# Kernel optimization log

Hardware: AMD Instinct MI355X
Metric: run time of the kernel (lower is better)

The kernel has to match this reference:

```python
import jax, jax.numpy as jnp
import numpy as np

N_E = 1024
E_DIM = 256
BETA = 0.25
DECAY = 0.99
EPS = 1e-5


def setup_inputs() -> dict:
    key = jax.random.key(0)
    k1, k2 = jax.random.split(key)
    z = jax.random.normal(k1, (16, E_DIM, 64, 64), dtype=jnp.float32)
    # embedding.weight.data.uniform_(-1/n_e, 1/n_e)
    weight = jax.random.uniform(k2, (N_E, E_DIM), dtype=jnp.float32,
                                minval=-1.0 / N_E, maxval=1.0 / N_E)
    cluster_size = jnp.zeros((N_E,), dtype=jnp.float32)
    embedding_avg = weight  # clone of initial weight
    return {"z": z, "weight": weight, "cluster_size": cluster_size,
            "embedding_avg": embedding_avg}


def reference(z, weight, cluster_size, embedding_avg):
    B, C, H, W = z.shape  # C == e_dim
    zp = jnp.transpose(z, (0, 2, 3, 1))          # [B,H,W,C]
    zf = zp.reshape(-1, C)                       # [N, C], N = B*H*W

    # ||z||^2 + ||e||^2 - 2 z e^T  -> [N, n_e]
    d = (jnp.sum(zf * zf, axis=1, keepdims=True)
         + jnp.sum(weight * weight, axis=1)
         - 2.0 * jnp.matmul(zf, weight.T))
    idx = jnp.argmin(d, axis=1)                  # [N] int

    z_q = weight[idx].reshape(zp.shape)          # [B,H,W,C]

    # EMA codebook update (training branch), computed with scatter-sums
    n_e = weight.shape[0]
    counts = jax.ops.segment_sum(jnp.ones(zf.shape[0], dtype=zf.dtype),
                                 idx, num_segments=n_e)        # encodings.sum(0)
    new_cluster_size = cluster_size * DECAY + (1.0 - DECAY) * counts
    n = jnp.sum(new_cluster_size)
    cs_smoothed = (new_cluster_size + EPS) / (n + n_e * EPS) * n
    dw = jax.ops.segment_sum(zf, idx, num_segments=n_e)        # encodings.T @ zf
    new_embedding_avg = embedding_avg * DECAY + (1.0 - DECAY) * dw
    new_weight = new_embedding_avg / cs_smoothed[:, None]

    loss = BETA * jnp.mean((jax.lax.stop_gradient(z_q) - zp) ** 2)
    z_q_st = zp + jax.lax.stop_gradient(z_q - zp)   # straight-through
    out = jnp.transpose(z_q_st, (0, 3, 1, 2))        # back to NCHW
    return out, loss, idx, new_cluster_size, new_embedding_avg, new_weight
```

## Files before the change

### kernel.cpp

```cpp
#include <hip/hip_runtime.h>
#include <hip/hip_bf16.h>

typedef unsigned short ushort_t;
typedef __attribute__((ext_vector_type(8))) _Float16 half8;
typedef __attribute__((ext_vector_type(4))) _Float16 half4;
typedef __attribute__((ext_vector_type(4))) float f32x4;

#define NB    16
#define NC    256
#define NHW   4096
#define NPIX  65536
#define NE    1024
#define BETA  0.25f
#define DECAY 0.99f
#define EPS_  1e-5f
#define GAP_FLAG 1.25e-4f

#define OFF_LOSS 16777216
#define OFF_IDXF 16777217
#define OFF_NCS  16842753
#define OFF_NEA  16843777
#define OFF_NW   17105921

#define WS_WSUM  0
#define WS_CSSM  1024
#define WS_LPART 2048
#define WS_CNT   4096
#define WS_FLAGS 4128
#define WS_LIST  6176
#define WS_WF16  40960
#define WS_ZF16  (WS_WF16 + 131072)
#define WS_IDXI  (WS_ZF16 + 8388608)
#define WS_CCNT  (WS_IDXI + 65536)
#define WS_OFFS  (WS_CCNT + 1024)
#define WS_CUR   (WS_OFFS + 1024)
#define WS_SORT  (WS_CUR + 1024)
#define WS_END   (WS_SORT + 65536)

__device__ __forceinline__ float sq_nofma(float x) {
    float s = x * x;
    asm volatile("" : "+v"(s));
    return s;
}

__device__ __forceinline__ float np_pair128_sq(const float* __restrict__ a) {
    float r[8];
    #pragma unroll
    for (int m = 0; m < 8; ++m) r[m] = sq_nofma(a[m]);
    for (int i = 8; i < 128; i += 8) {
        #pragma unroll
        for (int m = 0; m < 8; ++m) r[m] += sq_nofma(a[i + m]);
    }
    return ((r[0] + r[1]) + (r[2] + r[3])) + ((r[4] + r[5]) + (r[6] + r[7]));
}

__device__ __forceinline__ void gload16(const void* g, void* ldsp) {
    __builtin_amdgcn_global_load_lds((const __attribute__((address_space(1))) unsigned int*)g,
                                     (__attribute__((address_space(3))) unsigned int*)ldsp,
                                     16, 0, 0);
}

__global__ __launch_bounds__(64) void wsum_kernel(const float* __restrict__ w,
                                                  float* __restrict__ wsum,
                                                  float* __restrict__ ncs,
                                                  int* __restrict__ cnt,
                                                  int* __restrict__ ccount,
                                                  float* __restrict__ lpart) {
    int j = blockIdx.x * 64 + threadIdx.x;
    const float* wr = w + (size_t)j * NC;
    wsum[j] = np_pair128_sq(wr) + np_pair128_sq(wr + 128);
    ncs[j] = 0.0f;
    ccount[j] = 0;
    lpart[j] = 0.0f;
    lpart[j + 1024] = 0.0f;
    if (j == 0) cnt[0] = 0;
}

__global__ __launch_bounds__(256) void wpack_kernel(const float* __restrict__ w,
                                                    _Float16* __restrict__ wf) {
    int i = blockIdx.x * 256 + threadIdx.x;
    wf[i] = (_Float16)(w[i] * 1024.0f);
}

__global__ __launch_bounds__(256) void zpack_kernel(const float* __restrict__ z,
                                                    _Float16* __restrict__ zf) {
    __shared__ float zs[64 * 65];
    const int t = threadIdx.x;
    const int P0 = blockIdx.x * 64;
    const int b = P0 >> 12, hw0 = P0 & (NHW - 1);
    const int K0 = blockIdx.y * 64;
    const int hw = t & 63, cq = t >> 6;
    const float* zb = z + (size_t)b * (NC * NHW) + hw0 + hw;
    #pragma unroll
    for (int i = 0; i < 16; ++i) {
        int kl = cq * 16 + i;
        zs[hw * 65 + kl] = zb[(size_t)(K0 + kl) * NHW];
    }
    __syncthreads();
    const int p = t >> 2, kq = t & 3;
    size_t obase = (size_t)(P0 + p) * NC + K0 + kq * 16;
    #pragma unroll
    for (int h2 = 0; h2 < 2; ++h2) {
        half8 v;
        #pragma unroll
        for (int j2 = 0; j2 < 8; ++j2)
            v[j2] = (_Float16)zs[p * 65 + kq * 16 + h2 * 8 + j2];
        *(half8*)&zf[obase + h2 * 8] = v;
    }
}

__global__ __launch_bounds__(256) void gemm2_kernel(const _Float16* __restrict__ wf,
                                                    const _Float16* __restrict__ zf,
                                                    const float* __restrict__ wsum,
                                                    float* __restrict__ idxf,
                                                    int* __restrict__ idxi,
                                                    ushort_t* __restrict__ list,
                                                    int* __restrict__ cnt,
                                                    float* __restrict__ ncs,
                                                    int* __restrict__ ccount) {
    __shared__ __align__(16) char smem[81920];
    _Float16* zt = (_Float16*)smem;
    _Float16* wt = (_Float16*)(smem + 65536);
    float* bvx = (float*)(smem + 65536);
    float* svx = bvx + 256;
    int*   bix = (int*)(svx + 256);
    int*   h   = (int*)smem;

    const int t = threadIdx.x;
    const int l = t & 63;
    const int w = t >> 6;
    const int P0 = blockIdx.x * 128;
    const int wc = w >> 1, wp = w & 1;

    auto stage_w = [&](int ct, int ks, int buf) {
        #pragma unroll
        for (int i = 0; i < 2; ++i) {
            int row = w * 32 + i * 16 + (l >> 2);
            int gc = (l & 3) ^ ((l >> 3) & 3);
            gload16(wf + (size_t)(ct * 128 + row) * NC + ks * 32 + gc * 8,
                    &wt[buf * 4096 + w * 1024 + i * 512 + l * 8]);
        }
    };

    #pragma unroll
    for (int i = 0; i < 16; ++i) {
        int row = w * 32 + i * 2 + (l >> 5);
        int gc = (l & 31) ^ (row & 7);
        gload16(zf + (size_t)(P0 + row) * NC + gc * 8,
                &zt[w * 8192 + i * 512 + l * 8]);
    }
    stage_w(0, 0, 0);

    float rbv2[4], rsv2[4];
    int   rbi2[4];
    #pragma unroll
    for (int n = 0; n < 4; ++n) { rbv2[n] = 3.4e38f; rsv2[n] = 3.4e38f; rbi2[n] = 0; }

    __syncthreads();

    int buf = 0;
    for (int ct = 0; ct < 8; ++ct) {
        f32x4 acc[4][4];
        #pragma unroll
        for (int m = 0; m < 4; ++m)
            #pragma unroll
            for (int n = 0; n < 4; ++n)
                #pragma unroll
                for (int e = 0; e < 4; ++e) acc[m][n][e] = 0.0f;

        for (int ks = 0; ks < 8; ++ks) {
            int step = ct * 8 + ks;
            if (step < 63) {
                int ns = step + 1;
                stage_w(ns >> 3, ns & 7, buf ^ 1);
            }
            half8 a[4], b[4];
            #pragma unroll
            for (int m = 0; m < 4; ++m) {
                int row = wc * 64 + m * 16 + (l & 15);
                int g = (l >> 4) ^ ((row >> 1) & 3);
                a[m] = *(const half8*)&wt[buf * 4096 + row * 32 + g * 8];
            }
            #pragma unroll
            for (int n = 0; n < 4; ++n) {
                int row = wp * 64 + n * 16 + (l & 15);
                int chunk = (ks * 4 + (l >> 4)) ^ (row & 7);
                b[n] = *(const half8*)&zt[row * 256 + chunk * 8];
            }
            #pragma unroll
            for (int m = 0; m < 4; ++m)
                #pragma unroll
                for (int n = 0; n < 4; ++n)
                    acc[m][n] = __builtin_amdgcn_mfma_f32_16x16x32_f16(a[m], b[n], acc[m][n], 0, 0, 0);
            __syncthreads();
            buf ^= 1;
        }

        #pragma unroll
        for (int m = 0; m < 4; ++m) {
            float4 env = *(const float4*)&wsum[ct * 128 + wc * 64 + m * 16 + (l >> 4) * 4];
            const float* en = &env.x;
            #pragma unroll
            for (int n = 0; n < 4; ++n)
                #pragma unroll
                for (int r = 0; r < 4; ++r) {
                    float s = en[r] - acc[m][n][r] * 0.001953125f;
                    int code = ct * 128 + wc * 64 + m * 16 + (l >> 4) * 4 + r;
                    if (s < rbv2[n]) { rsv2[n] = rbv2[n]; rbv2[n] = s; rbi2[n] = code; }
                    else if (s < rsv2[n]) rsv2[n] = s;
                }
        }
    }

    #pragma unroll
    for (int n = 0; n < 4; ++n) {
        float bv = rbv2[n], sv = rsv2[n];
        int bi = rbi2[n];
        #pragma unroll
        for (int x = 16; x <= 32; x <<= 1) {
            float v2 = __shfl_xor(bv, x);
            float s2 = __shfl_xor(sv, x);
            int   i2 = __shfl_xor(bi, x);
            if (v2 < bv || (v2 == bv && i2 < bi)) { sv = fminf(bv, s2); bv = v2; bi = i2; }
            else sv = fminf(sv, v2);
        }
        if ((l >> 4) == 0) {
            int lp = wp * 64 + n * 16 + l;
            bvx[wc * 128 + lp] = bv;
            svx[wc * 128 + lp] = sv;
            bix[wc * 128 + lp] = bi;
        }
    }
    #pragma unroll
    for (int e = 0; e < 4; ++e) h[t + e * 256] = 0;
    __syncthreads();
    if (t < 128) {
        float bv = bvx[t], sv = svx[t];
        int bi = bix[t];
        float v2 = bvx[128 + t], s2 = svx[128 + t];
        int i2 = bix[128 + t];
        if (v2 < bv || (v2 == bv && i2 < bi)) { sv = fminf(bv, s2); bv = v2; bi = i2; }
        else sv = fminf(sv, v2);
        int pix = P0 + t;
        idxf[pix] = (float)bi;
        idxi[pix] = bi;
        atomicAdd(&h[bi], 1);
        if (sv - bv < GAP_FLAG) {
            int pos = atomicAdd(cnt, 1);
            list[pos] = (ushort_t)pix;
        }
    }
    __syncthreads();
    #pragma unroll
    for (int e = 0; e < 4; ++e) {
        int v = h[t + e * 256];
        if (v) {
            atomicAdd(&ncs[t + e * 256], (float)v);
            atomicAdd(&ccount[t + e * 256], v);
        }
    }
}

__global__ __launch_bounds__(256) void argmin_kernel(const float* __restrict__ z,
                                                     const float* __restrict__ w,
                                                     const float* __restrict__ enorm,
                                                     float* __restrict__ idxf,
                                                     int* __restrict__ idxi,
                                                     unsigned long long* __restrict__ flags) {
    __shared__ __align__(16) float smem[64 * 68 + 128 * 68];
    float* zt = smem;
    float* wt = smem + 64 * 68;
    const int t = threadIdx.x;
    const int pr = t & 7;
    const int cr = t >> 3;
    const int P0 = blockIdx.x * 64;
    const int b = P0 >> 12;
    const int hw0 = P0 & (NHW - 1);
    const float* zb = z + (size_t)b * (NC * NHW) + hw0;
    float bestv[8], secv[8];
    int besti[8];
    #pragma unroll
    for (int i = 0; i < 8; ++i) { bestv[i] = 3.4e38f; secv[i] = 3.4e38f; besti[i] = 0; }
    for (int cc = 0; cc < 8; ++cc) {
        float acc[8][4];
        #pragma unroll
        for (int i = 0; i < 8; ++i)
            #pragma unroll
            for (int j = 0; j < 4; ++j) acc[i][j] = 0.0f;
        for (int kc = 0; kc < 4; ++kc) {
            {
                int p = t & 63;
                int k0 = (t >> 6) * 16;
                int f2 = ((p >> 3) & 3) << 2;
                #pragma unroll
                for (int i = 0; i < 16; ++i) {
                    int k = k0 + i;
                    zt[p * 68 + (k ^ f2)] = zb[(size_t)(kc * 64 + k) * NHW + p];
                }
            }
            {
                #pragma unroll
                for (int i = 0; i < 8; ++i) {
                    int f = t + 256 * i;
                    int jj = f >> 4;
                    int k4 = f & 15;
                    float4 v = *(const float4*)&w[(size_t)(cc * 128 + jj) * NC + kc * 64 + k4 * 4];
                    *(float4*)&wt[jj * 68 + k4 * 4] = v;
                }
            }
            __syncthreads();
            #pragma unroll 2
            for (int k = 0; k < 64; k += 4) {
                float4 za[8], wb[4];
                #pragma unroll
                for (int i = 0; i < 8; ++i)
                    za[i] = *(float4*)&zt[(pr + 8 * i) * 68 + (k ^ ((i & 3) << 2))];
                #pragma unroll
                for (int j = 0; j < 4; ++j)
                    wb[j] = *(float4*)&wt[(cr + 32 * j) * 68 + k];
                #pragma unroll
                for (int i = 0; i < 8; ++i)
                    #pragma unroll
                    for (int j = 0; j < 4; ++j)
                        acc[i][j] += za[i].x * wb[j].x + za[i].y * wb[j].y +
                                     za[i].z * wb[j].z + za[i].w * wb[j].w;
            }
            __syncthreads();
        }
        #pragma unroll
        for (int j = 0; j < 4; ++j) {
            int code = cc * 128 + cr + 32 * j;
            float enj = enorm[code];
            #pragma unroll
            for (int i = 0; i < 8; ++i) {
                float s = enj - 2.0f * acc[i][j];
                if (s < bestv[i]) { secv[i] = bestv[i]; bestv[i] = s; besti[i] = code; }
                else if (s < secv[i]) secv[i] = s;
            }
        }
    }
    float* rv = smem;
    int* ri = (int*)(smem + 2048);
    float* rs = smem + 4096;
    #pragma unroll
    for (int i = 0; i < 8; ++i) {
        int p = pr + 8 * i;
        rv[p * 32 + cr] = bestv[i];
        ri[p * 32 + cr] = besti[i];
        rs[p * 32 + cr] = secv[i];
    }
    __syncthreads();
    if (t < 64) {
        int p = t;
        float bv = rv[p * 32], sv = rs[p * 32];
        int bi = ri[p * 32];
        for (int s2 = 1; s2 < 32; ++s2) {
            float v = rv[p * 32 + s2];
            float v2 = rs[p * 32 + s2];
            int ii = ri[p * 32 + s2];
            if (v < bv) { sv = bv; bv = v; bi = ii; }
            else {
                if (v < sv) sv = v;
                if (v == bv && ii < bi) bi = ii;
            }
            if (v2 < sv) sv = v2;
        }
        idxf[P0 + p] = (float)bi;
        idxi[P0 + p] = bi;
        unsigned long long mask = __ballot((sv - bv) < GAP_FLAG);
        if (t == 0) flags[blockIdx.x] = mask;
    }
}

__global__ __launch_bounds__(256) void gather_kernel(const unsigned long long* __restrict__ flags,
                                                     ushort_t* __restrict__ list,
                                                     int* __restrict__ cnt) {
    int p = blockIdx.x * 256 + threadIdx.x;
    unsigned long long m = flags[p >> 6];
    if ((m >> (p & 63)) & 1ULL) {
        int pos = atomicAdd(cnt, 1);
        list[pos] = (ushort_t)p;
    }
}

__global__ __launch_bounds__(1024) void hist_kernel(const int* __restrict__ idxi,
                                                    float* __restrict__ ncs) {
    __shared__ int h[NE];
    int t = threadIdx.x;
    h[t] = 0;
    __syncthreads();
    int gid = blockIdx.x * 1024 + t;
    #pragma unroll
    for (int i = 0; i < 4; ++i) atomicAdd(&h[idxi[gid + i * 16384]], 1);
    __syncthreads();
    if (h[t]) atomicAdd(&ncs[t], (float)h[t]);
}

__global__ __launch_bounds__(1024, 8) void dwloss_kernel(const float* __restrict__ z,
                                                         const float* __restrict__ w,
                                                         const int* __restrict__ idxi,
                                                         float* __restrict__ dw0,
                                                         float* __restrict__ dw1,
                                                         float* __restrict__ lpart) {
    __shared__ float acc[NE];
    __shared__ float wcol[NE];
    __shared__ float ls[16];
    const int c = blockIdx.x;
    const int part = blockIdx.y;
    const int t = threadIdx.x;
    acc[t] = 0.0f;
    wcol[t] = w[(size_t)t * NC + c];
    __syncthreads();
    const float* zc = z + (size_t)c * NHW;
    float lsum = 0.0f;
    #pragma unroll
    for (int half = 0; half < 2; ++half) {
        float4 zv[4];
        int4   iv[4];
        #pragma unroll
        for (int i = 0; i < 4; ++i) {
            int b = part * 8 + half * 4 + i;
            zv[i] = *(const float4*)&zc[(size_t)b * (NC * NHW) + t * 4];
            iv[i] = *(const int4*)&idxi[b * 4096 + t * 4];
        }
        #pragma unroll
        for (int i = 0; i < 4; ++i) {
            float q0 = wcol[iv[i].x], q1 = wcol[iv[i].y];
            float q2 = wcol[iv[i].z], q3 = wcol[iv[i].w];
            float d0 = q0 - zv[i].x, d1 = q1 - zv[i].y;
            float d2 = q2 - zv[i].z, d3 = q3 - zv[i].w;
            lsum += d0 * d0 + d1 * d1 + d2 * d2 + d3 * d3;
            atomicAdd(&acc[iv[i].x], zv[i].x);
            atomicAdd(&acc[iv[i].y], zv[i].y);
            atomicAdd(&acc[iv[i].z], zv[i].z);
            atomicAdd(&acc[iv[i].w], zv[i].w);
        }
    }
    #pragma unroll
    for (int off = 32; off > 0; off >>= 1) lsum += __shfl_down(lsum, off);
    if ((t & 63) == 0) ls[t >> 6] = lsum;
    __syncthreads();
    if (t == 0) {
        float s = 0.0f;
        #pragma unroll
        for (int q = 0; q < 16; ++q) s += ls[q];
        lpart[c * 2 + part] = s;
    }
    float* dwp = part ? dw1 : dw0;
    dwp[(size_t)t * NC + c] = acc[t];
}

__global__ __launch_bounds__(256) void fixup3_kernel(const float* __restrict__ z,
                                                     const float* __restrict__ w,
                                                     const float* __restrict__ wsum,
                                                     const ushort_t* __restrict__ list,
                                                     const int* __restrict__ cnt,
                                                     float* __restrict__ idxf,
                                                     int* __restrict__ idxi,
                                                     float* __restrict__ ncs,
                                                     int* __restrict__ ccount) {
    const int count = cnt[0];
    if (count == 0) return;
    const int ngroups = (count + 7) >> 3;
    const int t = threadIdx.x;

    __shared__ __align__(16) char smem_raw[16384 + 8192];
    double (*zd)[NC] = (double(*)[NC])smem_raw;
    float  (*zf)[NC] = (float(*)[NC])(smem_raw + 16384);
    float* rbv = (float*)(smem_raw + 16384);
    int*   rbi = (int*)smem_raw;
    __shared__ float zs_sh[8];
    __shared__ int   pix_sh[8];
    __shared__ float r2v[8][32];
    __shared__ int   r2i[8][32];

    for (int g = blockIdx.x; g < ngroups; g += gridDim.x) {
        if (t < 8) {
            int i = g * 8 + t;
            pix_sh[t] = (i < count) ? (int)list[i] : (int)list[0];
        }
        __syncthreads();
        #pragma unroll
        for (int px = 0; px < 8; ++px) {
            int p = pix_sh[px];
            int b = p >> 12, hw = p & (NHW - 1);
            float zv = z[(size_t)b * (NC * NHW) + (size_t)t * NHW + hw];
            zf[px][t] = zv;
            zd[px][t] = (double)zv;
        }
        __syncthreads();
        if (t < 8) zs_sh[t] = np_pair128_sq(zf[t]) + np_pair128_sq(zf[t] + 128);
        __syncthreads();

        float zs_reg[8];
        #pragma unroll
        for (int px = 0; px < 8; ++px) zs_reg[px] = zs_sh[px];

        float bvr[8];
        int   bir[8];
        #pragma unroll
        for (int px = 0; px < 8; ++px) { bvr[px] = 3.4e38f; bir[px] = 0; }

        #pragma unroll
        for (int jo = 0; jo < 2; ++jo) {
            const int j0 = t + jo * 512;
            const int j1 = j0 + 256;
            const float* wr0 = w + (size_t)j0 * NC;
            const float* wr1 = w + (size_t)j1 * NC;
            double acc0[8], acc1[8];
            #pragma unroll
            for (int px = 0; px < 8; ++px) { acc0[px] = 0.0; acc1[px] = 0.0; }
            for (int k = 0; k < NC; k += 4) {
                float4 wa = *(const float4*)&wr0[k];
                float4 wb = *(const float4*)&wr1[k];
                const float* wap = (const float*)&wa;
                const float* wbp = (const float*)&wb;
                #pragma unroll
                for (int e = 0; e < 4; ++e) {
                    double wea = (double)wap[e];
                    double web = (double)wbp[e];
                    #pragma unroll
                    for (int px = 0; px < 8; ++px) {
                        double zv = zd[px][k + e];
                        acc0[px] += wea * zv;
                        acc1[px] += web * zv;
                    }
                }
            }
            float ws0 = wsum[j0], ws1 = wsum[j1];
            #pragma unroll
            for (int px = 0; px < 8; ++px) {
                float m0 = (float)acc0[px];
                float s10 = zs_reg[px] + ws0;
                float d0 = s10 - 2.0f * m0;
                if (d0 < bvr[px] || (d0 == bvr[px] && j0 < bir[px])) { bvr[px] = d0; bir[px] = j0; }
                float m1 = (float)acc1[px];
                float s11 = zs_reg[px] + ws1;
                float d1 = s11 - 2.0f * m1;
                if (d1 < bvr[px] || (d1 == bvr[px] && j1 < bir[px])) { bvr[px] = d1; bir[px] = j1; }
            }
        }
        __syncthreads();
        #pragma unroll
        for (int px = 0; px < 8; ++px) {
            rbv[px * 256 + t] = bvr[px];
            rbi[px * 256 + t] = bir[px];
        }
        __syncthreads();
        {
            int px = t >> 5, s = t & 31;
            float bv = rbv[px * 256 + s * 8];
            int   bi = rbi[px * 256 + s * 8];
            #pragma unroll
            for (int e = 1; e < 8; ++e) {
                float v2 = rbv[px * 256 + s * 8 + e];
                int   i2 = rbi[px * 256 + s * 8 + e];
                if (v2 < bv || (v2 == bv && i2 < bi)) { bv = v2; bi = i2; }
            }
            r2v[px][s] = bv;
            r2i[px][s] = bi;
        }
        __syncthreads();
        if (t < 8) {
            float bv = r2v[t][0];
            int   bi = r2i[t][0];
            for (int s = 1; s < 32; ++s) {
                float v2 = r2v[t][s];
                int   i2 = r2i[t][s];
                if (v2 < bv || (v2 == bv && i2 < bi)) { bv = v2; bi = i2; }
            }
            if (g * 8 + t < count) {
                int p = pix_sh[t];
                int old = idxi[p];
                if (old != bi) {
                    idxf[p] = (float)bi;
                    idxi[p] = bi;
                    atomicAdd(&ncs[old], -1.0f);
                    atomicAdd(&ncs[bi], 1.0f);
                    if (ccount) {
                        atomicAdd(&ccount[old], -1);
                        atomicAdd(&ccount[bi], 1);
                    }
                }
            }
        }
        __syncthreads();
    }
}

__global__ __launch_bounds__(1024, 8) void out2_kernel(const float* __restrict__ w,
                                                       const int* __restrict__ idxi,
                                                       float* __restrict__ outq) {
    __shared__ float wcol[NE];
    const int c = blockIdx.x;
    const int part = blockIdx.y;
    const int t = threadIdx.x;
    wcol[t] = w[(size_t)t * NC + c];
    __syncthreads();
    float* oc = outq + (size_t)c * NHW;
    #pragma unroll
    for (int half = 0; half < 2; ++half) {
        int4 iv[4];
        #pragma unroll
        for (int i = 0; i < 4; ++i) {
            int b = part * 8 + half * 4 + i;
            iv[i] = *(const int4*)&idxi[b * 4096 + t * 4];
        }
        asm volatile("" :: "v"(iv[0].x), "v"(iv[1].x), "v"(iv[2].x), "v"(iv[3].x));
        #pragma unroll
        for (int i = 0; i < 4; ++i) {
            int b = part * 8 + half * 4 + i;
            float4 ov;
            ov.x = wcol[iv[i].x]; ov.y = wcol[iv[i].y];
            ov.z = wcol[iv[i].z]; ov.w = wcol[iv[i].w];
            *(float4*)&oc[(size_t)b * (NC * NHW) + t * 4] = ov;
        }
    }
}

__global__ __launch_bounds__(1024) void scan_kernel(const int* __restrict__ ccount,
                                                    int* __restrict__ offs,
                                                    int* __restrict__ cur) {
    __shared__ int s[1024];
    int t = threadIdx.x;
    int c0 = ccount[t];
    s[t] = c0;
    __syncthreads();
    for (int off = 1; off < 1024; off <<= 1) {
        int v = (t >= off) ? s[t - off] : 0;
        __syncthreads();
        s[t] += v;
        __syncthreads();
    }
    int ex = s[t] - c0;
    offs[t] = ex;
    cur[t] = ex;
}

__global__ __launch_bounds__(256) void scatter2_kernel(const int* __restrict__ idxi,
                                                       int* __restrict__ cur,
                                                       int* __restrict__ sorted) {
    int p = blockIdx.x * 256 + threadIdx.x;
    int id = idxi[p];
    int pos = atomicAdd(&cur[id], 1);
    sorted[pos] = p;
}

__global__ __launch_bounds__(256) void dwsum2_kernel(const _Float16* __restrict__ zf,
                                                     const float* __restrict__ w,
                                                     const int* __restrict__ sorted,
                                                     const int* __restrict__ offs,
                                                     const int* __restrict__ ccount,
                                                     float* __restrict__ dw0,
                                                     float* __restrict__ dw1,
                                                     float* __restrict__ lpart) {
    const int t = threadIdx.x, l = t & 63, wv = t >> 6;
    const int j = blockIdx.x * 4 + wv;
    const int part = blockIdx.y;
    const float4 q = *(const float4*)&w[(size_t)j * NC + l * 4];
    const int start = offs[j], cntj = ccount[j];
    const int h0 = (cntj + 1) >> 1;
    const int s = part ? start + h0 : start;
    const int e = part ? start + cntj : start + h0;
    float a0 = 0.f, a1 = 0.f, a2 = 0.f, a3 = 0.f, lsum = 0.f;
    for (int base = s; base < e; base += 64) {
        int pm = (base + l < e) ? sorted[base + l] : 0;
        int nn = min(64, e - base);
        for (int i = 0; i < nn; ++i) {
            int p = __shfl(pm, i);
            half4 zv = *(const half4*)&zf[(size_t)p * NC + l * 4];
            float z0 = (float)zv[0], z1 = (float)zv[1];
            float z2 = (float)zv[2], z3 = (float)zv[3];
            a0 += z0; a1 += z1; a2 += z2; a3 += z3;
            float d0 = q.x - z0, d1 = q.y - z1, d2 = q.z - z2, d3 = q.w - z3;
            lsum += d0 * d0 + d1 * d1 + d2 * d2 + d3 * d3;
        }
    }
    float* dwp = part ? dw1 : dw0;
    float4 av = make_float4(a0, a1, a2, a3);
    *(float4*)&dwp[(size_t)j * NC + l * 4] = av;
    #pragma unroll
    for (int off = 32; off > 0; off >>= 1) lsum += __shfl_down(lsum, off);
    if (l == 0) lpart[j * 2 + part] = lsum;
}

__global__ __launch_bounds__(1024) void finalize_kernel(const float* __restrict__ cs,
                                                        const float* __restrict__ lpart,
                                                        float* __restrict__ ncs,
                                                        float* __restrict__ cssm,
                                                        float* __restrict__ loss) {
    int t = threadIdx.x;
    float cnt = ncs[t];
    float v = cs[t] * DECAY + (1.0f - DECAY) * cnt;
    ncs[t] = v;
    __shared__ float red[1024];
    red[t] = v;
    __syncthreads();
    for (int s = 512; s > 0; s >>= 1) {
        if (t < s) red[t] += red[t + s];
        __syncthreads();
    }
    float n = red[0];
    __syncthreads();
    cssm[t] = (v + EPS_) / (n + (float)NE * EPS_) * n;
    red[t] = lpart[t] + lpart[t + 1024];
    __syncthreads();
    for (int s = 512; s > 0; s >>= 1) {
        if (t < s) red[t] += red[t + s];
        __syncthreads();
    }
    if (t == 0) loss[0] = BETA * red[0] / 16777216.0f;
}

__global__ __launch_bounds__(256) void neaw_kernel(const float* __restrict__ ea,
                                                   const float* __restrict__ cssm,
                                                   float* __restrict__ nea,
                                                   float* __restrict__ nw) {
    int lin = blockIdx.x * 256 + threadIdx.x;
    float dw = nea[lin] + nw[lin];
    float v = DECAY * ea[lin] + (1.0f - DECAY) * dw;
    nea[lin] = v;
    nw[lin] = v / cssm[lin >> 8];
}

extern "C" void kernel_launch(void* const* d_in, const int* in_sizes, int n_in,
                              void* d_out, int out_size, void* d_ws, size_t ws_size,
                              hipStream_t stream) {
    const float* z  = (const float*)d_in[0];
    const float* w  = (const float*)d_in[1];
    const float* cs = (const float*)d_in[2];
    const float* ea = (const float*)d_in[3];

    float* out  = (float*)d_out;
    float* loss = out + OFF_LOSS;
    float* idxf = out + OFF_IDXF;
    float* ncs  = out + OFF_NCS;
    float* nea  = out + OFF_NEA;
    float* nw   = out + OFF_NW;

    float* wsf = (float*)d_ws;
    float* wsum = wsf + WS_WSUM;
    float* cssm = wsf + WS_CSSM;
    float* lpart = wsf + WS_LPART;
    int* cnt = (int*)(wsf + WS_CNT);
    unsigned long long* flags = (unsigned long long*)(wsf + WS_FLAGS);
    ushort_t* list = (ushort_t*)(wsf + WS_LIST);
    int* idxi = (int*)(wsf + WS_IDXI);
    int* ccount = (int*)(wsf + WS_CCNT);
    int* offs = (int*)(wsf + WS_OFFS);
    int* cur = (int*)(wsf + WS_CUR);
    int* sorted = (int*)(wsf + WS_SORT);

    const bool fast = ws_size >= (size_t)WS_END * 4;

    hipLaunchKernelGGL(wsum_kernel, dim3(16), dim3(64), 0, stream, w, wsum, ncs, cnt,
                       fast ? ccount : cnt, lpart);

    if (fast) {
        _Float16* wf16 = (_Float16*)(wsf + WS_WF16);
        _Float16* zf16 = (_Float16*)(wsf + WS_ZF16);
        hipLaunchKernelGGL(wpack_kernel, dim3(1024), dim3(256), 0, stream, w, wf16);
        hipLaunchKernelGGL(zpack_kernel, dim3(1024, 4), dim3(256), 0, stream, z, zf16);
        hipLaunchKernelGGL(gemm2_kernel, dim3(512), dim3(256), 0, stream,
                           wf16, zf16, wsum, idxf, idxi, list, cnt, ncs, ccount);
        hipLaunchKernelGGL(fixup3_kernel, dim3(256), dim3(256), 0, stream,
                           z, w, wsum, list, cnt, idxf, idxi, ncs, ccount);
        hipLaunchKernelGGL(out2_kernel, dim3(256, 2), dim3(1024), 0, stream, w, idxi, out);
        hipLaunchKernelGGL(scan_kernel, dim3(1), dim3(1024), 0, stream, ccount, offs, cur);
        hipLaunchKernelGGL(scatter2_kernel, dim3(256), dim3(256), 0, stream, idxi, cur, sorted);
        hipLaunchKernelGGL(dwsum2_kernel, dim3(256, 2), dim3(256), 0, stream,
                           zf16, w, sorted, offs, ccount, nea, nw, lpart);
    } else {
        hipLaunchKernelGGL(argmin_kernel, dim3(1024), dim3(256), 0, stream, z, w, wsum, idxf, idxi, flags);
        hipLaunchKernelGGL(gather_kernel, dim3(256), dim3(256), 0, stream, flags, list, cnt);
        hipLaunchKernelGGL(hist_kernel, dim3(16), dim3(1024), 0, stream, idxi, ncs);
        hipLaunchKernelGGL(fixup3_kernel, dim3(256), dim3(256), 0, stream,
                           z, w, wsum, list, cnt, idxf, idxi, ncs, (int*)nullptr);
        hipLaunchKernelGGL(out2_kernel, dim3(256, 2), dim3(1024), 0, stream, w, idxi, out);
        hipLaunchKernelGGL(dwloss_kernel, dim3(256, 2), dim3(1024), 0, stream, z, w, idxi, nea, nw, lpart);
    }

    hipLaunchKernelGGL(finalize_kernel, dim3(1), dim3(1024), 0, stream, cs, lpart, ncs, cssm, loss);
    hipLaunchKernelGGL(neaw_kernel, dim3(1024), dim3(256), 0, stream, ea, cssm, nea, nw);
}
```

Baseline: 256.1 us.

## Enlarge gemm2 pixel tile to 256 with 512-thread blocks and precomputed offsets

The distance GEMM block now covers 256 pixels with 8 waves instead of 128 pixels with 4 waves, so each staged codebook tile is reused across twice as many pixels and global W traffic per pixel halves. LDS addressing is precomputed outside the k-loop, the k-loop is fully unrolled, and s_setprio raises wave priority around the MFMA section. LDS grows to 144KB, which allows one block per CU, and the grid shrinks to 256 blocks, which may leave some CUs idle and reduce latency hiding.

```diff
diff --git a/kernel.cpp b/kernel.cpp
--- a/kernel.cpp
+++ b/kernel.cpp
@@ -109,7 +109,7 @@
     }
 }
 
-__global__ __launch_bounds__(256) void gemm2_kernel(const _Float16* __restrict__ wf,
+__global__ __launch_bounds__(512) void gemm2_kernel(const _Float16* __restrict__ wf,
                                                     const _Float16* __restrict__ zf,
                                                     const float* __restrict__ wsum,
                                                     float* __restrict__ idxf,
@@ -118,29 +118,39 @@
                                                     int* __restrict__ cnt,
                                                     float* __restrict__ ncs,
                                                     int* __restrict__ ccount) {
-    __shared__ __align__(16) char smem[81920];
+    __shared__ __align__(16) char smem[147456];
     _Float16* zt = (_Float16*)smem;
-    _Float16* wt = (_Float16*)(smem + 65536);
-    float* bvx = (float*)(smem + 65536);
-    float* svx = bvx + 256;
-    int*   bix = (int*)(svx + 256);
+    _Float16* wt = (_Float16*)(smem + 131072);
+    float* bvx = (float*)(smem + 131072);
+    float* svx = bvx + 512;
+    int*   bix = (int*)(svx + 512);
     int*   h   = (int*)smem;
 
     const int t = threadIdx.x;
     const int l = t & 63;
     const int w = t >> 6;
-    const int P0 = blockIdx.x * 128;
-    const int wc = w >> 1, wp = w & 1;
-
-    auto stage_w = [&](int ct, int ks, int buf) {
-        #pragma unroll
-        for (int i = 0; i < 2; ++i) {
-            int row = w * 32 + i * 16 + (l >> 2);
-            int gc = (l & 3) ^ ((l >> 3) & 3);
-            gload16(wf + (size_t)(ct * 128 + row) * NC + ks * 32 + gc * 8,
-                    &wt[buf * 4096 + w * 1024 + i * 512 + l * 8]);
-        }
-    };
+    const int P0 = blockIdx.x * 256;
+    const int wc = w >> 2;
+    const int wp = w & 3;
+
+    const int sdest = w * 512 + l * 8;
+    const int swrow = w * 16 + (l >> 2);
+    const _Float16* wsrc0 = wf + (size_t)swrow * 256 + (((l & 3) ^ ((l >> 3) & 3)) * 8);
+    int aoff[4];
+    #pragma unroll
+    for (int m = 0; m < 4; ++m) {
+        int row = wc * 64 + m * 16 + (l & 15);
+        int g = (l >> 4) ^ ((row >> 1) & 3);
+        aoff[m] = row * 32 + g * 8;
+    }
+    int bbase[4], bx32[4];
+    #pragma unroll
+    for (int n = 0; n < 4; ++n) {
+        int row = wp * 64 + n * 16 + (l & 15);
+        int r3 = row & 7;
+        bbase[n] = row * 256 + (((l >> 4) ^ (r3 & 3)) * 8);
+        bx32[n] = (r3 >> 2) * 32;
+    }
 
     #pragma unroll
     for (int i = 0; i < 16; ++i) {
@@ -149,7 +159,7 @@
         gload16(zf + (size_t)(P0 + row) * NC + gc * 8,
                 &zt[w * 8192 + i * 512 + l * 8]);
     }
-    stage_w(0, 0, 0);
+    gload16(wsrc0, &wt[sdest]);
 
     float rbv2[4], rsv2[4];
     int   rbi2[4];
@@ -158,8 +168,8 @@
 
     __syncthreads();
 
-    int buf = 0;
     for (int ct = 0; ct < 8; ++ct) {
+        const _Float16* wsrc_ct = wsrc0 + ct * 32768;
         f32x4 acc[4][4];
         #pragma unroll
         for (int m = 0; m < 4; ++m)
@@ -168,32 +178,28 @@
                 #pragma unroll
                 for (int e = 0; e < 4; ++e) acc[m][n][e] = 0.0f;
 
+        #pragma unroll
         for (int ks = 0; ks < 8; ++ks) {
-            int step = ct * 8 + ks;
-            if (step < 63) {
-                int ns = step + 1;
-                stage_w(ns >> 3, ns & 7, buf ^ 1);
-            }
+            if (ct < 7 || ks < 7) {
+                const _Float16* src = (ks < 7) ? (wsrc_ct + (ks + 1) * 32)
+                                               : (wsrc_ct + 32768);
+                gload16(src, &wt[((ks & 1) ^ 1) * 4096 + sdest]);
+            }
+            __builtin_amdgcn_s_setprio(1);
             half8 a[4], b[4];
             #pragma unroll
-            for (int m = 0; m < 4; ++m) {
-                int row = wc * 64 + m * 16 + (l & 15);
-                int g = (l >> 4) ^ ((row >> 1) & 3);
-                a[m] = *(const half8*)&wt[buf * 4096 + row * 32 + g * 8];
-            }
-            #pragma unroll
-            for (int n = 0; n < 4; ++n) {
-                int row = wp * 64 + n * 16 + (l & 15);
-                int chunk = (ks * 4 + (l >> 4)) ^ (row & 7);
-                b[n] = *(const half8*)&zt[row * 256 + chunk * 8];
-            }
+            for (int m = 0; m < 4; ++m)
+                a[m] = *(const half8*)&wt[(ks & 1) * 4096 + aoff[m]];
+            #pragma unroll
+            for (int n = 0; n < 4; ++n)
+                b[n] = *(const half8*)&zt[bbase[n] + ((ks * 32) ^ bx32[n])];
             #pragma unroll
             for (int m = 0; m < 4; ++m)
                 #pragma unroll
                 for (int n = 0; n < 4; ++n)
                     acc[m][n] = __builtin_amdgcn_mfma_f32_16x16x32_f16(a[m], b[n], acc[m][n], 0, 0, 0);
+            __builtin_amdgcn_s_setprio(0);
             __syncthreads();
-            buf ^= 1;
         }
 
         #pragma unroll
@@ -226,19 +232,19 @@
         }
         if ((l >> 4) == 0) {
             int lp = wp * 64 + n * 16 + l;
-            bvx[wc * 128 + lp] = bv;
-            svx[wc * 128 + lp] = sv;
-            bix[wc * 128 + lp] = bi;
-        }
-    }
-    #pragma unroll
-    for (int e = 0; e < 4; ++e) h[t + e * 256] = 0;
-    __syncthreads();
-    if (t < 128) {
+            bvx[wc * 256 + lp] = bv;
+            svx[wc * 256 + lp] = sv;
+            bix[wc * 256 + lp] = bi;
+        }
+    }
+    h[t] = 0;
+    h[t + 512] = 0;
+    __syncthreads();
+    if (t < 256) {
         float bv = bvx[t], sv = svx[t];
         int bi = bix[t];
-        float v2 = bvx[128 + t], s2 = svx[128 + t];
-        int i2 = bix[128 + t];
+        float v2 = bvx[256 + t], s2 = svx[256 + t];
+        int i2 = bix[256 + t];
         if (v2 < bv || (v2 == bv && i2 < bi)) { sv = fminf(bv, s2); bv = v2; bi = i2; }
         else sv = fminf(sv, v2);
         int pix = P0 + t;
@@ -251,13 +257,11 @@
         }
     }
     __syncthreads();
-    #pragma unroll
-    for (int e = 0; e < 4; ++e) {
-        int v = h[t + e * 256];
-        if (v) {
-            atomicAdd(&ncs[t + e * 256], (float)v);
-            atomicAdd(&ccount[t + e * 256], v);
-        }
+    {
+        int v = h[t];
+        if (v) { atomicAdd(&ncs[t], (float)v); atomicAdd(&ccount[t], v); }
+        v = h[t + 512];
+        if (v) { atomicAdd(&ncs[t + 512], (float)v); atomicAdd(&ccount[t + 512], v); }
     }
 }
 
@@ -761,7 +765,7 @@
         _Float16* zf16 = (_Float16*)(wsf + WS_ZF16);
         hipLaunchKernelGGL(wpack_kernel, dim3(1024), dim3(256), 0, stream, w, wf16);
         hipLaunchKernelGGL(zpack_kernel, dim3(1024, 4), dim3(256), 0, stream, z, zf16);
-        hipLaunchKernelGGL(gemm2_kernel, dim3(512), dim3(256), 0, stream,
+        hipLaunchKernelGGL(gemm2_kernel, dim3(256), dim3(512), 0, stream,
                            wf16, zf16, wsum, idxf, idxi, list, cnt, ncs, ccount);
         hipLaunchKernelGGL(fixup3_kernel, dim3(256), dim3(256), 0, stream,
                            z, w, wsum, list, cnt, idxf, idxi, ncs, ccount);
```

Measured after the change: 260.0 us. About the same (+1.5%).
